# Optimization experiments

Measured on AMD Instinct MI355X. Metric: run time of the kernel, lower is better.

## Reference

```python
import jax, jax.numpy as jnp
import numpy as np

EPS = 1e-5


def ternarize(w):
    # TWN: delta = 0.7*mean|w|; alpha = mean of |w| over entries above delta
    delta = 0.7 * jnp.mean(jnp.abs(w))
    mask = (jnp.abs(w) > delta).astype(w.dtype)
    alpha = jnp.sum(jnp.abs(w) * mask) / jnp.maximum(jnp.sum(mask), 1.0)
    q = alpha * jnp.sign(w) * mask
    # straight-through estimator (matches torch `w + (q - w).detach()`)
    return w + jax.lax.stop_gradient(q - w)


def conv2d(x, w, stride, pad):
    # x: NCHW, w: OIHW
    return jax.lax.conv_general_dilated(
        x, w, window_strides=(stride, stride), padding=[(pad, pad), (pad, pad)],
        dimension_numbers=("NCHW", "OIHW", "NCHW"))


def batchnorm(x, gamma, beta, mean, var):
    # inference-mode BN over channel dim of NCHW
    inv = gamma / jnp.sqrt(var + EPS)
    return x * inv[None, :, None, None] + (beta - mean * inv)[None, :, None, None]


def setup_inputs() -> dict:
    key = jax.random.key(0)
    ks = jax.random.split(key, 12)
    d = {
        "x": jax.random.normal(ks[0], (64, 3, 224, 224), jnp.float32),
        "w1": jax.random.normal(ks[1], (32, 3, 3, 3), jnp.float32) * 0.1,
        "g1": jnp.ones((32,), jnp.float32), "b1": jnp.zeros((32,), jnp.float32),
        "m1": jax.random.normal(ks[2], (32,), jnp.float32) * 0.1,
        "v1": jax.random.uniform(ks[3], (32,), jnp.float32, 0.5, 1.5),
        "w2": jax.random.normal(ks[4], (64, 32, 3, 3), jnp.float32) * 0.05,
        "g2": jnp.ones((64,), jnp.float32), "b2": jnp.zeros((64,), jnp.float32),
        "m2": jax.random.normal(ks[5], (64,), jnp.float32) * 0.1,
        "v2": jax.random.uniform(ks[6], (64,), jnp.float32, 0.5, 1.5),
        "w3": jax.random.normal(ks[7], (128, 64, 3, 3), jnp.float32) * 0.05,
        "g3": jnp.ones((128,), jnp.float32), "b3": jnp.zeros((128,), jnp.float32),
        "m3": jax.random.normal(ks[8], (128,), jnp.float32) * 0.1,
        "v3": jax.random.uniform(ks[9], (128,), jnp.float32, 0.5, 1.5),
        "wl": jax.random.normal(ks[10], (10, 128), jnp.float32) * 0.1,
        "bl": jax.random.normal(ks[11], (10,), jnp.float32) * 0.01,
    }
    return d


def reference(x, w1, g1, b1, m1, v1, w2, g2, b2, m2, v2,
              w3, g3, b3, m3, v3, wl, bl):
    h = jax.nn.relu(batchnorm(conv2d(x, ternarize(w1), 2, 1), g1, b1, m1, v1))
    h = jax.nn.relu(batchnorm(conv2d(h, ternarize(w2), 1, 1), g2, b2, m2, v2))
    h = jax.nn.relu(batchnorm(conv2d(h, ternarize(w3), 2, 1), g3, b3, m3, v3))
    h = jnp.mean(h, axis=(2, 3))  # AdaptiveAvgPool2d((1,1)) + flatten -> [N,128]
    return h @ ternarize(wl).T + bl
```

## Files before the change

### kernel.cpp

```cpp
#include <hip/hip_runtime.h>
#include <cstddef>

typedef __attribute__((ext_vector_type(8))) short short8;
typedef __attribute__((ext_vector_type(4))) float floatx4;

__device__ __forceinline__ unsigned short f2bf(float f) {
  union { float f; unsigned u; } v; v.f = f;
  const unsigned r = v.u + 0x7fffu + ((v.u >> 16) & 1u);
  return (unsigned short)(r >> 16);
}

__device__ __forceinline__ float block_reduce_sum(float v, float* sm) {
#pragma unroll
  for (int off = 32; off > 0; off >>= 1) v += __shfl_down(v, off, 64);
  const int lane = threadIdx.x & 63, wid = threadIdx.x >> 6;
  __syncthreads();
  if (lane == 0) sm[wid] = v;
  __syncthreads();
  if (threadIdx.x == 0) {
    float t = 0.f;
    const int nw = (blockDim.x + 63) >> 6;
    for (int i = 0; i < nw; ++i) t += sm[i];
    sm[0] = t;
  }
  __syncthreads();
  return sm[0];
}

__device__ __forceinline__ void tsel(int t, const float* w0, const float* w1,
                                     const float* w2, const float* w3, int n0,
                                     int n1, int n2, int n3,
                                     const float*& w, int& n) {
  w = (t == 0) ? w0 : (t == 1) ? w1 : (t == 2) ? w2 : w3;
  n = (t == 0) ? n0 : (t == 1) ? n1 : (t == 2) ? n2 : n3;
}

__global__ __launch_bounds__(256) void tern_phase1(
    const float* w0, const float* w1, const float* w2, const float* w3,
    int n0, int n1, int n2, int n3, float* __restrict__ red) {
  __shared__ float sm[8];
  const float* w; int n;
  tsel(blockIdx.y, w0, w1, w2, w3, n0, n1, n2, n3, w, n);
  if ((int)blockIdx.x * 256 >= n) return;
  const int i = blockIdx.x * 256 + threadIdx.x;
  float s = (i < n) ? fabsf(w[i]) : 0.f;
  s = block_reduce_sum(s, sm);
  if (threadIdx.x == 0) atomicAdd(&red[blockIdx.y * 4 + 0], s);
}

__global__ __launch_bounds__(256) void tern_phase2(
    const float* w0, const float* w1, const float* w2, const float* w3,
    int n0, int n1, int n2, int n3, float* __restrict__ red,
    unsigned short* __restrict__ bp1, unsigned short* __restrict__ bp2,
    unsigned short* __restrict__ bp3, float* __restrict__ ql) {
  __shared__ float sm[8];
  const float* w; int n;
  const int by = blockIdx.y;
  tsel(by, w0, w1, w2, w3, n0, n1, n2, n3, w, n);
  if ((int)blockIdx.x * 256 >= n) return;
  const float delta = 0.7f * red[by * 4 + 0] / (float)n;
  const int i = blockIdx.x * 256 + threadIdx.x;
  float c = 0.f, a = 0.f;
  float wv = 0.f;
  if (i < n) {
    wv = w[i];
    const float av = fabsf(wv);
    if (av > delta) { c = 1.f; a = av; }
  }
  if (i < n) {
    const float sgnf = (wv > delta) ? 1.f : (wv < -delta ? -1.f : 0.f);
    const unsigned short sgnb =
        (wv > delta) ? 0x3F80u : (wv < -delta ? 0xBF80u : 0u);
    if (by == 0) {
      const int k = i % 27, oc = i / 27;
      bp1[((size_t)(k >> 3) * 32 + oc) * 8 + (k & 7)] = sgnb;
    } else if (by == 1) {
      const int k = (i % 9) * 32 + (i % 288) / 9;
      bp2[((size_t)(k >> 3) * 64 + i / 288) * 8 + (k & 7)] = sgnb;
    } else if (by == 2) {
      const int k = (i % 9) * 64 + (i % 576) / 9;
      bp3[((size_t)(k >> 3) * 128 + i / 576) * 8 + (k & 7)] = sgnb;
    } else {
      ql[i] = sgnf;
    }
  }
  c = block_reduce_sum(c, sm);
  a = block_reduce_sum(a, sm);
  if (threadIdx.x == 0) {
    atomicAdd(&red[by * 4 + 1], c);
    atomicAdd(&red[by * 4 + 2], a);
  }
}

__global__ void bnfold_all(
    const float* g1, const float* b1, const float* m1, const float* v1,
    const float* g2, const float* b2, const float* m2, const float* v2,
    const float* g3, const float* b3, const float* m3, const float* v3,
    float* s1, float* bb1, float* s2, float* bb2, float* s3, float* bb3,
    const float* __restrict__ red) {
  const int i = threadIdx.x;
  if (i < 32) {
    const float inv = g1[i] / sqrtf(v1[i] + 1e-5f);
    const float a = red[2] / fmaxf(red[1], 1.f);
    s1[i] = a * inv; bb1[i] = b1[i] - m1[i] * inv;
  } else if (i < 96) {
    const int c = i - 32;
    const float inv = g2[c] / sqrtf(v2[c] + 1e-5f);
    const float a = red[6] / fmaxf(red[5], 1.f);
    s2[c] = a * inv; bb2[c] = b2[c] - m2[c] * inv;
  } else if (i < 224) {
    const int c = i - 96;
    const float inv = g3[c] / sqrtf(v3[c] + 1e-5f);
    const float a = red[10] / fmaxf(red[9], 1.f);
    s3[c] = a * inv; bb3[c] = b3[c] - m3[c] * inv;
  }
}

__global__ __launch_bounds__(256) void conv1_mfma(
    const float* __restrict__ x, const unsigned short* __restrict__ bp1,
    const float* __restrict__ s1, const float* __restrict__ bb1,
    unsigned short* __restrict__ y) {
  __shared__ float xs[3 * 17 * 33];
  __shared__ unsigned short im[128 * 40];
  const int n = blockIdx.y;
  const int oh0 = (blockIdx.x / 7) * 8, ow0 = (blockIdx.x % 7) * 16;
  const int t = threadIdx.x;
  const int wave = t >> 6, lane = t & 63, quad = lane >> 4, l16 = lane & 15;

  const int ihb = oh0 * 2 - 1, iwb = ow0 * 2 - 1;
  for (int i = t; i < 1683; i += 256) {
    const int ic = i / 561, r2 = i % 561;
    const int pr = r2 / 33, pc = r2 % 33;
    const int ih = ihb + pr, iw = iwb + pc;
    float v = 0.f;
    if ((unsigned)ih < 224u && (unsigned)iw < 224u)
      v = x[((size_t)n * 3 + ic) * 50176 + (size_t)ih * 224 + iw];
    xs[i] = v;
  }
  __syncthreads();

#pragma unroll
  for (int cc = 0; cc < 2; ++cc) {
    const int c = cc * 256 + t;
    const int px = c >> 2, seg = c & 3;
    const int ohl = px >> 4, owl = px & 15;
    unsigned u[4];
#pragma unroll
    for (int jj = 0; jj < 4; ++jj) {
      unsigned short lo = 0, hi = 0;
      const int k0 = seg * 8 + 2 * jj, k1 = k0 + 1;
      if (k0 < 27) {
        const int ic = k0 / 9, tp = k0 % 9;
        lo = f2bf(xs[(ic * 17 + ohl * 2 + tp / 3) * 33 + owl * 2 + tp % 3]);
      }
      if (k1 < 27) {
        const int ic = k1 / 9, tp = k1 % 9;
        hi = f2bf(xs[(ic * 17 + ohl * 2 + tp / 3) * 33 + owl * 2 + tp % 3]);
      }
      u[jj] = (unsigned)lo | ((unsigned)hi << 16);
    }
    *(uint4*)(&im[px * 40 + seg * 8]) = make_uint4(u[0], u[1], u[2], u[3]);
  }

  short8 bfr[2];
#pragma unroll
  for (int nf = 0; nf < 2; ++nf)
    bfr[nf] = *(const short8*)(bp1 + ((size_t)quad * 32 + nf * 16 + l16) * 8);

  floatx4 acc[2][2];
#pragma unroll
  for (int mi = 0; mi < 2; ++mi) {
    acc[mi][0] = (floatx4){0.f, 0.f, 0.f, 0.f};
    acc[mi][1] = (floatx4){0.f, 0.f, 0.f, 0.f};
  }
  __syncthreads();

#pragma unroll
  for (int mi = 0; mi < 2; ++mi) {
    const int pxb = (wave * 2 + mi) * 16;
    const short8 a = *(const short8*)(&im[(pxb + l16) * 40 + quad * 8]);
#pragma unroll
    for (int nf = 0; nf < 2; ++nf)
      acc[mi][nf] = __builtin_amdgcn_mfma_f32_16x16x32_bf16(
          a, bfr[nf], acc[mi][nf], 0, 0, 0);
  }

  float sc[2], bs[2];
#pragma unroll
  for (int nf = 0; nf < 2; ++nf) {
    sc[nf] = s1[nf * 16 + l16];
    bs[nf] = bb1[nf * 16 + l16];
  }
#pragma unroll
  for (int mi = 0; mi < 2; ++mi) {
    const int oh = oh0 + wave * 2 + mi;
#pragma unroll
    for (int r = 0; r < 4; ++r) {
      const int ow = ow0 + quad * 4 + r;
      const size_t base = (((size_t)n * 112 + oh) * 112 + ow) * 32;
#pragma unroll
      for (int nf = 0; nf < 2; ++nf) {
        const float vv = fmaxf(acc[mi][nf][r] * sc[nf] + bs[nf], 0.f);
        y[base + nf * 16 + l16] = f2bf(vv);
      }
    }
  }
}

__global__ __launch_bounds__(256) void conv2_halo(
    const unsigned short* __restrict__ xin,
    const unsigned short* __restrict__ bp,
    const float* __restrict__ scale, const float* __restrict__ bias,
    unsigned short* __restrict__ yout) {
  constexpr int PH = 10, PW = 18;
  __shared__ unsigned short patch[4 * PH * PW * 8];
  const int t = threadIdx.x;
  const int img = blockIdx.z;
  const int toh = blockIdx.x / 7, tow = blockIdx.x % 7;
  const int wave = t >> 6, lane = t & 63, quad = lane >> 4, l16 = lane & 15;
  const int oh0 = toh * 8, ow0 = tow * 16;

  for (int c = t; c < PH * PW * 4; c += 256) {
    const int pix = c >> 2, seg = c & 3;
    const int pi = pix / PW, pj = pix % PW;
    const int ih = oh0 - 1 + pi, iw = ow0 - 1 + pj;
    uint4 v = make_uint4(0u, 0u, 0u, 0u);
    if ((unsigned)ih < 112u && (unsigned)iw < 112u)
      v = *(const uint4*)(xin + (((size_t)img * 112 + ih) * 112 + iw) * 32 +
                          seg * 8);
    *(uint4*)(&patch[((seg * PH + pi) * PW + pj) * 8]) = v;
  }

  floatx4 acc[2][4];
#pragma unroll
  for (int mf = 0; mf < 2; ++mf)
#pragma unroll
    for (int nf = 0; nf < 4; ++nf) acc[mf][nf] = (floatx4){0.f, 0.f, 0.f, 0.f};

  short8 bcur[4], bnxt[4];
#pragma unroll
  for (int nf = 0; nf < 4; ++nf)
    bcur[nf] = *(const short8*)(bp + ((size_t)quad * 64 + nf * 16 + l16) * 8);
  __syncthreads();

#pragma unroll
  for (int tap = 0; tap < 9; ++tap) {
    const int kh = tap / 3, kw = tap % 3;
    if (tap + 1 < 9) {
      const int kg = (tap + 1) * 4 + quad;
#pragma unroll
      for (int nf = 0; nf < 4; ++nf)
        bnxt[nf] = *(const short8*)(bp + ((size_t)kg * 64 + nf * 16 + l16) * 8);
    }
#pragma unroll
    for (int mf = 0; mf < 2; ++mf) {
      const int pi = (wave * 2 + mf) + kh;
      const short8 a = *(const short8*)(
          &patch[((quad * PH + pi) * PW + l16 + kw) * 8]);
#pragma unroll
      for (int nf = 0; nf < 4; ++nf)
        acc[mf][nf] = __builtin_amdgcn_mfma_f32_16x16x32_bf16(
            a, bcur[nf], acc[mf][nf], 0, 0, 0);
    }
#pragma unroll
    for (int nf = 0; nf < 4; ++nf) bcur[nf] = bnxt[nf];
  }

  float sc[4], bs[4];
#pragma unroll
  for (int nf = 0; nf < 4; ++nf) {
    sc[nf] = scale[nf * 16 + l16];
    bs[nf] = bias[nf * 16 + l16];
  }
#pragma unroll
  for (int mf = 0; mf < 2; ++mf) {
    const int oh = oh0 + wave * 2 + mf;
#pragma unroll
    for (int r = 0; r < 4; ++r) {
      const int ow = ow0 + quad * 4 + r;
      const size_t base = (((size_t)img * 112 + oh) * 112 + ow) * 64;
#pragma unroll
      for (int nf = 0; nf < 4; ++nf) {
        const float vv = fmaxf(acc[mf][nf][r] * sc[nf] + bs[nf], 0.f);
        yout[base + nf * 16 + l16] = f2bf(vv);
      }
    }
  }
}

__global__ __launch_bounds__(256, 5) void conv3_pool(
    const unsigned short* __restrict__ act2,
    const unsigned short* __restrict__ bp3,
    const float* __restrict__ s3, const float* __restrict__ bb3,
    float* __restrict__ pooled) {
  __shared__ unsigned short c2p[4 * 17 * 18 * 8];
  __shared__ float pbuf[128];
  const int t = threadIdx.x;
  const int img = blockIdx.y;
  const int ty = blockIdx.x / 7, tx = blockIdx.x % 7;
  const int o3h0 = ty * 8, o3w0 = tx * 8;
  const int wave = t >> 6, lane = t & 63, quad = lane >> 4, l16 = lane & 15;

  int a3off[4];
#pragma unroll
  for (int mf = 0; mf < 4; ++mf) {
    const int px = mf * 16 + l16;
    a3off[mf] = ((quad * 17 + (px >> 3) * 2) * 18 + (px & 7)) * 8;
  }

  floatx4 acc3[4][2];
#pragma unroll
  for (int mf = 0; mf < 4; ++mf) {
    acc3[mf][0] = (floatx4){0.f, 0.f, 0.f, 0.f};
    acc3[mf][1] = (floatx4){0.f, 0.f, 0.f, 0.f};
  }

  const int h0 = o3h0 * 2 - 1, w0 = o3w0 * 2 - 1;
#pragma unroll
  for (int h = 0; h < 2; ++h) {
    if (h) __syncthreads();
    for (int c = t; c < 17 * 17 * 4; c += 256) {
      const int pix = c >> 2, seg = c & 3;
      const int pi = pix / 17, pj = pix % 17;
      const int ih = h0 + pi, iw = w0 + pj;
      uint4 v = make_uint4(0u, 0u, 0u, 0u);
      if ((unsigned)ih < 112u && (unsigned)iw < 112u)
        v = *(const uint4*)(act2 + (((size_t)img * 112 + ih) * 112 + iw) * 64 +
                            h * 32 + seg * 8);
      const int slot = (pj >> 1) + (pj & 1) * 9;
      *(uint4*)(&c2p[((seg * 17 + pi) * 18 + slot) * 8]) = v;
    }
    __syncthreads();
#pragma unroll
    for (int tap = 0; tap < 9; ++tap) {
      const int kh = tap / 3, kw = tap % 3;
      const int kg = tap * 8 + h * 4 + quad;
      const short8 b0 = *(const short8*)(
          bp3 + ((size_t)kg * 128 + wave * 32 + l16) * 8);
      const short8 b1 = *(const short8*)(
          bp3 + ((size_t)kg * 128 + wave * 32 + 16 + l16) * 8);
      const int toff = (kh * 18 + (kw >> 1) + (kw & 1) * 9) * 8;
#pragma unroll
      for (int mf = 0; mf < 4; ++mf) {
        const short8 a = *(const short8*)(&c2p[a3off[mf] + toff]);
        acc3[mf][0] = __builtin_amdgcn_mfma_f32_16x16x32_bf16(
            a, b0, acc3[mf][0], 0, 0, 0);
        acc3[mf][1] = __builtin_amdgcn_mfma_f32_16x16x32_bf16(
            a, b1, acc3[mf][1], 0, 0, 0);
      }
    }
  }

#pragma unroll
  for (int nf = 0; nf < 2; ++nf) {
    const int ch = wave * 32 + nf * 16 + l16;
    const float sc = s3[ch], bs = bb3[ch];
    float s = 0.f;
#pragma unroll
    for (int mf = 0; mf < 4; ++mf)
#pragma unroll
      for (int r = 0; r < 4; ++r)
        s += fmaxf(acc3[mf][nf][r] * sc + bs, 0.f);
    s += __shfl_xor(s, 16);
    s += __shfl_xor(s, 32);
    if (lane < 16) pbuf[ch] = s;
  }
  __syncthreads();
  if (t < 128) atomicAdd(&pooled[(size_t)img * 128 + t], pbuf[t]);
}

__global__ void linear_kernel(const float* __restrict__ pooled,
                              const float* __restrict__ ql,
                              const float* __restrict__ bl,
                              const float* __restrict__ red,
                              float* __restrict__ out) {
  const int idx = blockIdx.x * blockDim.x + threadIdx.x;
  if (idx >= 64 * 10) return;
  const int n = idx / 10, o = idx % 10;
  const float* p = pooled + (size_t)n * 128;
  const float* w = ql + (size_t)o * 128;
  float s = 0.f;
#pragma unroll 4
  for (int c = 0; c < 128; ++c) s += p[c] * w[c];
  const float alpha_l = red[14] / fmaxf(red[13], 1.f);
  out[idx] = s * (alpha_l / 3136.f) + bl[o];
}

extern "C" void kernel_launch(void* const* d_in, const int* in_sizes, int n_in,
                              void* d_out, int out_size, void* d_ws,
                              size_t ws_size, hipStream_t stream) {
  const float* x  = (const float*)d_in[0];
  const float* w1 = (const float*)d_in[1];
  const float* g1 = (const float*)d_in[2];
  const float* b1 = (const float*)d_in[3];
  const float* m1 = (const float*)d_in[4];
  const float* v1 = (const float*)d_in[5];
  const float* w2 = (const float*)d_in[6];
  const float* g2 = (const float*)d_in[7];
  const float* b2 = (const float*)d_in[8];
  const float* m2 = (const float*)d_in[9];
  const float* v2 = (const float*)d_in[10];
  const float* w3 = (const float*)d_in[11];
  const float* g3 = (const float*)d_in[12];
  const float* b3 = (const float*)d_in[13];
  const float* m3 = (const float*)d_in[14];
  const float* v3 = (const float*)d_in[15];
  const float* wl = (const float*)d_in[16];
  const float* bl = (const float*)d_in[17];
  float* out = (float*)d_out;

  float* Wf = (float*)d_ws;
  float* red = Wf;
  float* pooled = red + 16;
  float* bp1f = pooled + 8192;
  float* ql = bp1f + 512;
  float* s1 = ql + 1280;  float* bb1 = s1 + 32;
  float* s2 = bb1 + 32;   float* bb2 = s2 + 64;
  float* s3 = bb2 + 64;   float* bb3 = s3 + 128;
  unsigned short* bp1 = (unsigned short*)bp1f;
  unsigned short* Us = (unsigned short*)(bb3 + 128);
  unsigned short* bp2 = Us;
  unsigned short* bp3 = bp2 + 18432;
  unsigned short* act1 = bp3 + 73728;
  unsigned short* act2 = act1 + 25690112;

  hipMemsetAsync(red, 0, (16 + 8192 + 512) * sizeof(float), stream);
  tern_phase1<<<dim3(288, 4), 256, 0, stream>>>(w1, w2, w3, wl, 864, 18432,
                                                73728, 1280, red);
  tern_phase2<<<dim3(288, 4), 256, 0, stream>>>(w1, w2, w3, wl, 864, 18432,
                                                73728, 1280, red, bp1, bp2,
                                                bp3, ql);
  bnfold_all<<<1, 256, 0, stream>>>(g1, b1, m1, v1, g2, b2, m2, v2, g3, b3,
                                    m3, v3, s1, bb1, s2, bb2, s3, bb3, red);

  conv1_mfma<<<dim3(98, 64), 256, 0, stream>>>(x, bp1, s1, bb1, act1);
  conv2_halo<<<dim3(98, 1, 64), 256, 0, stream>>>(act1, bp2, s2, bb2, act2);
  conv3_pool<<<dim3(49, 64), 256, 0, stream>>>(act2, bp3, s3, bb3, pooled);
  linear_kernel<<<3, 256, 0, stream>>>(pooled, ql, bl, red, out);
}
```

Baseline: 259.3 us.

## Fold BN into conv epilogues and double-buffer conv3 channel-half loads

Removes the separate bnfold_all launch; each conv kernel now computes its BN scale and bias from gamma, beta, mean, var and the ternary alpha in its epilogue. conv3_pool switches to two LDS buffers. The global loads for the second channel half are issued into registers before the MFMA work on the first half, so their latency overlaps that compute. The extra LDS and register pressure lower the launch-bounds occupancy hint from 5 to 4 blocks per CU, and the BN math is redone in every block.

```diff
diff --git a/kernel.cpp b/kernel.cpp
--- a/kernel.cpp
+++ b/kernel.cpp
@@ -92,34 +92,11 @@
   }
 }
 
-__global__ void bnfold_all(
-    const float* g1, const float* b1, const float* m1, const float* v1,
-    const float* g2, const float* b2, const float* m2, const float* v2,
-    const float* g3, const float* b3, const float* m3, const float* v3,
-    float* s1, float* bb1, float* s2, float* bb2, float* s3, float* bb3,
-    const float* __restrict__ red) {
-  const int i = threadIdx.x;
-  if (i < 32) {
-    const float inv = g1[i] / sqrtf(v1[i] + 1e-5f);
-    const float a = red[2] / fmaxf(red[1], 1.f);
-    s1[i] = a * inv; bb1[i] = b1[i] - m1[i] * inv;
-  } else if (i < 96) {
-    const int c = i - 32;
-    const float inv = g2[c] / sqrtf(v2[c] + 1e-5f);
-    const float a = red[6] / fmaxf(red[5], 1.f);
-    s2[c] = a * inv; bb2[c] = b2[c] - m2[c] * inv;
-  } else if (i < 224) {
-    const int c = i - 96;
-    const float inv = g3[c] / sqrtf(v3[c] + 1e-5f);
-    const float a = red[10] / fmaxf(red[9], 1.f);
-    s3[c] = a * inv; bb3[c] = b3[c] - m3[c] * inv;
-  }
-}
-
 __global__ __launch_bounds__(256) void conv1_mfma(
     const float* __restrict__ x, const unsigned short* __restrict__ bp1,
-    const float* __restrict__ s1, const float* __restrict__ bb1,
-    unsigned short* __restrict__ y) {
+    const float* __restrict__ g1, const float* __restrict__ b1,
+    const float* __restrict__ m1, const float* __restrict__ v1,
+    const float* __restrict__ red, unsigned short* __restrict__ y) {
   __shared__ float xs[3 * 17 * 33];
   __shared__ unsigned short im[128 * 40];
   const int n = blockIdx.y;
@@ -185,11 +162,14 @@
           a, bfr[nf], acc[mi][nf], 0, 0, 0);
   }
 
+  const float alpha1 = red[2] / fmaxf(red[1], 1.f);
   float sc[2], bs[2];
 #pragma unroll
   for (int nf = 0; nf < 2; ++nf) {
-    sc[nf] = s1[nf * 16 + l16];
-    bs[nf] = bb1[nf * 16 + l16];
+    const int ch = nf * 16 + l16;
+    const float inv = g1[ch] / sqrtf(v1[ch] + 1e-5f);
+    sc[nf] = alpha1 * inv;
+    bs[nf] = b1[ch] - m1[ch] * inv;
   }
 #pragma unroll
   for (int mi = 0; mi < 2; ++mi) {
@@ -210,8 +190,9 @@
 __global__ __launch_bounds__(256) void conv2_halo(
     const unsigned short* __restrict__ xin,
     const unsigned short* __restrict__ bp,
-    const float* __restrict__ scale, const float* __restrict__ bias,
-    unsigned short* __restrict__ yout) {
+    const float* __restrict__ g2, const float* __restrict__ b2,
+    const float* __restrict__ m2, const float* __restrict__ v2,
+    const float* __restrict__ red, unsigned short* __restrict__ yout) {
   constexpr int PH = 10, PW = 18;
   __shared__ unsigned short patch[4 * PH * PW * 8];
   const int t = threadIdx.x;
@@ -266,11 +247,14 @@
     for (int nf = 0; nf < 4; ++nf) bcur[nf] = bnxt[nf];
   }
 
+  const float alpha2 = red[6] / fmaxf(red[5], 1.f);
   float sc[4], bs[4];
 #pragma unroll
   for (int nf = 0; nf < 4; ++nf) {
-    sc[nf] = scale[nf * 16 + l16];
-    bs[nf] = bias[nf * 16 + l16];
+    const int ch = nf * 16 + l16;
+    const float inv = g2[ch] / sqrtf(v2[ch] + 1e-5f);
+    sc[nf] = alpha2 * inv;
+    bs[nf] = b2[ch] - m2[ch] * inv;
   }
 #pragma unroll
   for (int mf = 0; mf < 2; ++mf) {
@@ -288,18 +272,20 @@
   }
 }
 
-__global__ __launch_bounds__(256, 5) void conv3_pool(
+__global__ __launch_bounds__(256, 4) void conv3_pool(
     const unsigned short* __restrict__ act2,
     const unsigned short* __restrict__ bp3,
-    const float* __restrict__ s3, const float* __restrict__ bb3,
-    float* __restrict__ pooled) {
-  __shared__ unsigned short c2p[4 * 17 * 18 * 8];
+    const float* __restrict__ g3, const float* __restrict__ b3,
+    const float* __restrict__ m3, const float* __restrict__ v3,
+    const float* __restrict__ red, float* __restrict__ pooled) {
+  __shared__ unsigned short c2p[2][4 * 17 * 18 * 8];
   __shared__ float pbuf[128];
   const int t = threadIdx.x;
   const int img = blockIdx.y;
   const int ty = blockIdx.x / 7, tx = blockIdx.x % 7;
   const int o3h0 = ty * 8, o3w0 = tx * 8;
   const int wave = t >> 6, lane = t & 63, quad = lane >> 4, l16 = lane & 15;
+  const int h0 = o3h0 * 2 - 1, w0 = o3w0 * 2 - 1;
 
   int a3off[4];
 #pragma unroll
@@ -315,58 +301,86 @@
     acc3[mf][1] = (floatx4){0.f, 0.f, 0.f, 0.f};
   }
 
-  const int h0 = o3h0 * 2 - 1, w0 = o3w0 * 2 - 1;
-#pragma unroll
-  for (int h = 0; h < 2; ++h) {
-    if (h) __syncthreads();
-    for (int c = t; c < 17 * 17 * 4; c += 256) {
-      const int pix = c >> 2, seg = c & 3;
-      const int pi = pix / 17, pj = pix % 17;
-      const int ih = h0 + pi, iw = w0 + pj;
-      uint4 v = make_uint4(0u, 0u, 0u, 0u);
-      if ((unsigned)ih < 112u && (unsigned)iw < 112u)
-        v = *(const uint4*)(act2 + (((size_t)img * 112 + ih) * 112 + iw) * 64 +
-                            h * 32 + seg * 8);
-      const int slot = (pj >> 1) + (pj & 1) * 9;
-      *(uint4*)(&c2p[((seg * 17 + pi) * 18 + slot) * 8]) = v;
-    }
-    __syncthreads();
-#pragma unroll
-    for (int tap = 0; tap < 9; ++tap) {
-      const int kh = tap / 3, kw = tap % 3;
-      const int kg = tap * 8 + h * 4 + quad;
-      const short8 b0 = *(const short8*)(
-          bp3 + ((size_t)kg * 128 + wave * 32 + l16) * 8);
-      const short8 b1 = *(const short8*)(
-          bp3 + ((size_t)kg * 128 + wave * 32 + 16 + l16) * 8);
-      const int toff = (kh * 18 + (kw >> 1) + (kw & 1) * 9) * 8;
-#pragma unroll
-      for (int mf = 0; mf < 4; ++mf) {
-        const short8 a = *(const short8*)(&c2p[a3off[mf] + toff]);
-        acc3[mf][0] = __builtin_amdgcn_mfma_f32_16x16x32_bf16(
-            a, b0, acc3[mf][0], 0, 0, 0);
-        acc3[mf][1] = __builtin_amdgcn_mfma_f32_16x16x32_bf16(
-            a, b1, acc3[mf][1], 0, 0, 0);
-      }
-    }
-  }
-
+  uint4 r[5];
+#define C3_ISSUE(H)                                                          \
+  {                                                                          \
+    _Pragma("unroll") for (int i = 0; i < 5; ++i) {                          \
+      const int c = i * 256 + t;                                             \
+      uint4 v = make_uint4(0u, 0u, 0u, 0u);                                  \
+      if (c < 1156) {                                                        \
+        const int pix = c >> 2, seg = c & 3;                                 \
+        const int pi = pix / 17, pj = pix % 17;                              \
+        const int ih = h0 + pi, iw = w0 + pj;                                \
+        if ((unsigned)ih < 112u && (unsigned)iw < 112u)                      \
+          v = *(const uint4*)(act2 +                                         \
+                              (((size_t)img * 112 + ih) * 112 + iw) * 64 +   \
+                              (H) * 32 + seg * 8);                           \
+      }                                                                      \
+      r[i] = v;                                                              \
+    }                                                                        \
+  }
+#define C3_WRITE(H)                                                          \
+  {                                                                          \
+    _Pragma("unroll") for (int i = 0; i < 5; ++i) {                          \
+      const int c = i * 256 + t;                                             \
+      if (c < 1156) {                                                        \
+        const int pix = c >> 2, seg = c & 3;                                 \
+        const int pi = pix / 17, pj = pix % 17;                              \
+        const int slot = (pj >> 1) + (pj & 1) * 9;                           \
+        *(uint4*)(&c2p[H][((seg * 17 + pi) * 18 + slot) * 8]) = r[i];        \
+      }                                                                      \
+    }                                                                        \
+  }
+#define C3_COMPUTE(H)                                                        \
+  {                                                                          \
+    _Pragma("unroll") for (int tap = 0; tap < 9; ++tap) {                    \
+      const int kh = tap / 3, kw = tap % 3;                                  \
+      const int kg = tap * 8 + (H) * 4 + quad;                               \
+      const short8 b0 =                                                      \
+          *(const short8*)(bp3 + ((size_t)kg * 128 + wave * 32 + l16) * 8);  \
+      const short8 b1 = *(const short8*)(bp3 + ((size_t)kg * 128 +           \
+                                                wave * 32 + 16 + l16) * 8);  \
+      const int toff = (kh * 18 + (kw >> 1) + (kw & 1) * 9) * 8;             \
+      _Pragma("unroll") for (int mf = 0; mf < 4; ++mf) {                     \
+        const short8 a = *(const short8*)(&c2p[H][a3off[mf] + toff]);        \
+        acc3[mf][0] = __builtin_amdgcn_mfma_f32_16x16x32_bf16(               \
+            a, b0, acc3[mf][0], 0, 0, 0);                                    \
+        acc3[mf][1] = __builtin_amdgcn_mfma_f32_16x16x32_bf16(               \
+            a, b1, acc3[mf][1], 0, 0, 0);                                    \
+      }                                                                      \
+    }                                                                        \
+  }
+
+  C3_ISSUE(0);
+  C3_WRITE(0);
+  __syncthreads();
+  C3_ISSUE(1);
+  C3_COMPUTE(0);
+  C3_WRITE(1);
+  __syncthreads();
+  C3_COMPUTE(1);
+
+  const float alpha3 = red[10] / fmaxf(red[9], 1.f);
 #pragma unroll
   for (int nf = 0; nf < 2; ++nf) {
     const int ch = wave * 32 + nf * 16 + l16;
-    const float sc = s3[ch], bs = bb3[ch];
+    const float inv = g3[ch] / sqrtf(v3[ch] + 1e-5f);
+    const float sc = alpha3 * inv, bs = b3[ch] - m3[ch] * inv;
     float s = 0.f;
 #pragma unroll
     for (int mf = 0; mf < 4; ++mf)
 #pragma unroll
-      for (int r = 0; r < 4; ++r)
-        s += fmaxf(acc3[mf][nf][r] * sc + bs, 0.f);
+      for (int rr = 0; rr < 4; ++rr)
+        s += fmaxf(acc3[mf][nf][rr] * sc + bs, 0.f);
     s += __shfl_xor(s, 16);
     s += __shfl_xor(s, 32);
     if (lane < 16) pbuf[ch] = s;
   }
   __syncthreads();
   if (t < 128) atomicAdd(&pooled[(size_t)img * 128 + t], pbuf[t]);
+#undef C3_ISSUE
+#undef C3_WRITE
+#undef C3_COMPUTE
 }
 
 __global__ void linear_kernel(const float* __restrict__ pooled,
@@ -414,11 +428,8 @@
   float* pooled = red + 16;
   float* bp1f = pooled + 8192;
   float* ql = bp1f + 512;
-  float* s1 = ql + 1280;  float* bb1 = s1 + 32;
-  float* s2 = bb1 + 32;   float* bb2 = s2 + 64;
-  float* s3 = bb2 + 64;   float* bb3 = s3 + 128;
   unsigned short* bp1 = (unsigned short*)bp1f;
-  unsigned short* Us = (unsigned short*)(bb3 + 128);
+  unsigned short* Us = (unsigned short*)(ql + 1280);
   unsigned short* bp2 = Us;
   unsigned short* bp3 = bp2 + 18432;
   unsigned short* act1 = bp3 + 73728;
@@ -430,11 +441,12 @@
   tern_phase2<<<dim3(288, 4), 256, 0, stream>>>(w1, w2, w3, wl, 864, 18432,
                                                 73728, 1280, red, bp1, bp2,
                                                 bp3, ql);
-  bnfold_all<<<1, 256, 0, stream>>>(g1, b1, m1, v1, g2, b2, m2, v2, g3, b3,
-                                    m3, v3, s1, bb1, s2, bb2, s3, bb3, red);
-
-  conv1_mfma<<<dim3(98, 64), 256, 0, stream>>>(x, bp1, s1, bb1, act1);
-  conv2_halo<<<dim3(98, 1, 64), 256, 0, stream>>>(act1, bp2, s2, bb2, act2);
-  conv3_pool<<<dim3(49, 64), 256, 0, stream>>>(act2, bp3, s3, bb3, pooled);
+
+  conv1_mfma<<<dim3(98, 64), 256, 0, stream>>>(x, bp1, g1, b1, m1, v1, red,
+                                               act1);
+  conv2_halo<<<dim3(98, 1, 64), 256, 0, stream>>>(act1, bp2, g2, b2, m2, v2,
+                                                  red, act2);
+  conv3_pool<<<dim3(49, 64), 256, 0, stream>>>(act2, bp3, g3, b3, m3, v3, red,
+                                               pooled);
   linear_kernel<<<3, 256, 0, stream>>>(pooled, ql, bl, red, out);
 }
```

New measurement: 265.4 us. 1.02x slower.
